# Kernel tuning notes

Hardware: AMD Instinct MI355X
Metric: run time of the kernel (lower is better)

Reference implementation:

```python
import jax, jax.numpy as jnp
import numpy as np

N = 50000
NEG_SLOPE = 0.2  # PyG GATConv default leaky_relu slope


def _gat_layer(x, src, dst, W, a_s, a_d, b):
    # x: [N, Fin]; W: [Fin, H*C]; a_s, a_d: [H, C]; b: [C]
    H, C = a_s.shape
    xp = (x @ W).reshape(N, H, C)                      # projected node features per head
    alpha_s = jnp.einsum('nhc,hc->nh', xp, a_s)        # [N, H]
    alpha_d = jnp.einsum('nhc,hc->nh', xp, a_d)        # [N, H]
    e = jax.nn.leaky_relu(alpha_s[src] + alpha_d[dst], NEG_SLOPE)  # [E, H]
    # segment softmax over incoming edges of each dst node
    m = jax.ops.segment_max(e, dst, num_segments=N)
    m = jnp.where(jnp.isfinite(m), m, 0.0)
    p = jnp.exp(e - jax.lax.stop_gradient(m)[dst])
    denom = jax.ops.segment_sum(p, dst, num_segments=N)
    alpha = p / denom[dst]                             # [E, H]
    # scatter-aggregate messages
    out = jax.ops.segment_sum(alpha[:, :, None] * xp[src], dst, num_segments=N)  # [N, H, C]
    return out.mean(axis=1) + b                        # concat=False -> mean over heads


def setup_inputs() -> dict:
    key = jax.random.key(0)
    ks = jax.random.split(key, 16)
    IN, HID, OUT, H = 128, 64, 40, 4
    E = 800000
    x = jax.random.normal(ks[0], (N, IN), dtype=jnp.float32)
    edge_index = jax.random.randint(ks[1], (2, E), 0, N, dtype=jnp.int64)

    def mk(kw, ka, fin, fout):
        s = 1.0 / np.sqrt(fin)
        W = jax.random.normal(kw, (fin, H * fout), dtype=jnp.float32) * s
        a_s = jax.random.normal(ka, (H, fout), dtype=jnp.float32) * 0.1
        a_d = jax.random.normal(jax.random.fold_in(ka, 1), (H, fout), dtype=jnp.float32) * 0.1
        b = jnp.zeros((fout,), dtype=jnp.float32)
        return W, a_s, a_d, b

    W1, as1, ad1, b1 = mk(ks[2], ks[3], IN, HID)
    W2, as2, ad2, b2 = mk(ks[4], ks[5], HID, HID)
    W3, as3, ad3, b3 = mk(ks[6], ks[7], HID, OUT)
    return dict(x=x, edge_index=edge_index,
                W1=W1, as1=as1, ad1=ad1, b1=b1,
                W2=W2, as2=as2, ad2=ad2, b2=b2,
                W3=W3, as3=as3, ad3=ad3, b3=b3)


def reference(x, edge_index, W1, as1, ad1, b1, W2, as2, ad2, b2, W3, as3, ad3, b3):
    # PyG GATConv adds self-loops by default
    loop = jnp.arange(N, dtype=edge_index.dtype)
    src = jnp.concatenate([edge_index[0], loop])
    dst = jnp.concatenate([edge_index[1], loop])
    h = jax.nn.relu(_gat_layer(x, src, dst, W1, as1, ad1, b1))   # dropout is identity in eval
    h = jax.nn.relu(_gat_layer(h, src, dst, W2, as2, ad2, b2))
    h = jax.nn.relu(_gat_layer(h, src, dst, W3, as3, ad3, b3))
    return jax.nn.log_softmax(h, axis=-1)
```

## Files before the change

kernel.cpp:

```cpp
#include <hip/hip_runtime.h>
#include <math.h>

#define NNODES 50000
#define NEG_SLOPE 0.2f

typedef unsigned short ushort8v __attribute__((ext_vector_type(8)));
typedef unsigned short ushort4v __attribute__((ext_vector_type(4)));
typedef short short8v __attribute__((ext_vector_type(8)));
typedef float f32x4 __attribute__((ext_vector_type(4)));
typedef float f32x2 __attribute__((ext_vector_type(2)));

__device__ __forceinline__ unsigned short f2bf(float f){
    unsigned u = __float_as_uint(f);
    u += 0x7fff + ((u >> 16) & 1);
    return (unsigned short)(u >> 16);
}

__global__ void init_kernel(const unsigned long long* __restrict__ e, int* __restrict__ flag,
                            int* __restrict__ deg, int N){
    if(blockIdx.x == 0 && threadIdx.x < 64){
        const unsigned long long v = e[threadIdx.x];
        const unsigned long long mask = __ballot(v >= (1ULL << 32));
        if(threadIdx.x == 0) *flag = (mask == 0ULL) ? 1 : 0;
    }
    for(int i = blockIdx.x * blockDim.x + threadIdx.x; i < N; i += gridDim.x * blockDim.x)
        deg[i] = 0;
}

__global__ void hist_kernel(const void* __restrict__ e, const int* __restrict__ flag,
                            int* __restrict__ deg, int E){
    const int i = blockIdx.x * blockDim.x + threadIdx.x;
    if(i < E){
        const int d = (*flag) ? (int)((const long long*)e)[E + i] : ((const int*)e)[E + i];
        atomicAdd(&deg[d], 1);
    }
}

__global__ __launch_bounds__(512) void scan1_kernel(const int* __restrict__ deg,
                                                    int* __restrict__ excl,
                                                    int* __restrict__ bsum, int n){
    __shared__ int sh[512];
    const int t = threadIdx.x;
    const int gid = blockIdx.x * 512 + t;
    const int v = (gid < n) ? deg[gid] : 0;
    sh[t] = v;
    __syncthreads();
    for(int off = 1; off < 512; off <<= 1){
        const int add = (t >= off) ? sh[t - off] : 0;
        __syncthreads();
        sh[t] += add;
        __syncthreads();
    }
    if(gid < n) excl[gid] = sh[t] - v;
    if(t == 511) bsum[blockIdx.x] = sh[511];
}

__global__ __launch_bounds__(128) void scan2_kernel(int* __restrict__ bsum, int nb){
    __shared__ int sh[128];
    const int t = threadIdx.x;
    const int v = (t < nb) ? bsum[t] : 0;
    sh[t] = v;
    __syncthreads();
    for(int off = 1; off < 128; off <<= 1){
        const int add = (t >= off) ? sh[t - off] : 0;
        __syncthreads();
        sh[t] += add;
        __syncthreads();
    }
    if(t < nb) bsum[t] = sh[t] - v;
}

__global__ void scan3_kernel(const int* __restrict__ excl, const int* __restrict__ bsum,
                             int* __restrict__ row_ptr, int* __restrict__ cursor,
                             int n, int E){
    const int gid = blockIdx.x * blockDim.x + threadIdx.x;
    if(gid < n){
        const int r = excl[gid] + bsum[gid >> 9];
        row_ptr[gid] = r;
        cursor[gid] = r;
    }
    if(gid == 0) row_ptr[n] = E;
}

__global__ void scatter_kernel(const void* __restrict__ e, const int* __restrict__ flag,
                               int* __restrict__ cursor, int* __restrict__ col, int E){
    const int i = blockIdx.x * blockDim.x + threadIdx.x;
    if(i < E){
        int s, d;
        if(*flag){ s = (int)((const long long*)e)[i]; d = (int)((const long long*)e)[E + i]; }
        else     { s = ((const int*)e)[i];            d = ((const int*)e)[E + i]; }
        const int pos = atomicAdd(&cursor[d], 1);
        col[pos] = s;
    }
}

__device__ __forceinline__ void emit_wa(const float* __restrict__ W, const float* __restrict__ a_s,
                                        const float* __restrict__ a_d, unsigned short* __restrict__ Wt,
                                        int Kin, int C, int id){
    const int n = id / Kin, k = id - n * Kin;
    float v = 0.f;
    if(n < 8){
        const int hh = n & 3;
        const float* av = (n < 4) ? a_s : a_d;
        for(int c = 0; c < C; c++) v += W[(size_t)k * (4 * C) + hh * C + c] * av[hh * C + c];
    }
    Wt[id] = f2bf(v);
}

__device__ __forceinline__ void emit_wc(const float* __restrict__ W, unsigned short* __restrict__ Wt,
                                        int Kin, int C, int id){
    const int c = id / (4 * Kin);
    const int hk = id - c * (4 * Kin);
    const int h = hk / Kin, k = hk - h * Kin;
    const float v = (c < C) ? W[(size_t)k * (4 * C) + h * C + c] * 0.25f : 0.f;
    Wt[id] = f2bf(v);
}

__global__ void prep_kernel(const float* __restrict__ x, unsigned short* __restrict__ xbf, int X4,
                            const float* __restrict__ W1, const float* __restrict__ as1, const float* __restrict__ ad1,
                            const float* __restrict__ W2, const float* __restrict__ as2, const float* __restrict__ ad2,
                            const float* __restrict__ W3, const float* __restrict__ as3, const float* __restrict__ ad3,
                            unsigned short* __restrict__ Wa1, unsigned short* __restrict__ Wa2,
                            unsigned short* __restrict__ Wa3, unsigned short* __restrict__ Wc1,
                            unsigned short* __restrict__ Wc2, unsigned short* __restrict__ Wc3){
    int id = blockIdx.x * blockDim.x + threadIdx.x;
    if(id < X4){
        const float4 v = *(const float4*)&x[(size_t)id * 4];
        ushort4v o;
        o[0] = f2bf(v.x); o[1] = f2bf(v.y); o[2] = f2bf(v.z); o[3] = f2bf(v.w);
        *(ushort4v*)&xbf[(size_t)id * 4] = o;
        return;
    }
    id -= X4;
    if(id < 16 * 128){ emit_wa(W1, as1, ad1, Wa1, 128, 64, id); return; }
    id -= 16 * 128;
    if(id < 16 * 64){ emit_wa(W2, as2, ad2, Wa2, 64, 64, id); return; }
    id -= 16 * 64;
    if(id < 16 * 64){ emit_wa(W3, as3, ad3, Wa3, 64, 40, id); return; }
    id -= 16 * 64;
    if(id < 64 * 512){ emit_wc(W1, Wc1, 128, 64, id); return; }
    id -= 64 * 512;
    if(id < 64 * 256){ emit_wc(W2, Wc2, 64, 64, id); return; }
    id -= 64 * 256;
    if(id < 48 * 256){ emit_wc(W3, Wc3, 64, 40, id); }
}

template<int K>
__global__ __launch_bounds__(256) void agemm_kernel(const unsigned short* __restrict__ A,
                                                    const unsigned short* __restrict__ Wa,
                                                    float* __restrict__ ea, float* __restrict__ ed,
                                                    int M){
    const int lane = threadIdx.x & 63;
    const int wave = threadIdx.x >> 6;
    const int quad = lane >> 4;
    const int l16 = lane & 15;
    const int bm = blockIdx.x * 64;
    const int m = min(bm + wave * 16 + l16, M - 1);
    f32x4 acc = {0,0,0,0};
    #pragma unroll
    for(int k0 = 0; k0 < K; k0 += 32){
        const short8v a = *(const short8v*)&A[(size_t)m * K + k0 + quad * 8];
        const short8v b = *(const short8v*)&Wa[(size_t)l16 * K + k0 + quad * 8];
        acc = __builtin_amdgcn_mfma_f32_16x16x32_bf16(a, b, acc, 0, 0, 0);
    }
    if(l16 < 8){
        const int h = l16 & 3;
        float* dst = (l16 < 4) ? ea : ed;
        const int rbase = bm + wave * 16 + quad * 4;
        #pragma unroll
        for(int r = 0; r < 4; r++){
            const int row = rbase + r;
            if(row < M){
                const float v = acc[r];
                *(f32x2*)&dst[(size_t)row * 8 + 2 * h] = (f32x2){__expf(v), __expf(NEG_SLOPE * v)};
            }
        }
    }
}

template<int K>
__global__ __launch_bounds__(256) void gather_kernel(const unsigned short* __restrict__ X,
                                                     const int* __restrict__ row_ptr,
                                                     const int* __restrict__ col,
                                                     const float* __restrict__ ea,
                                                     const float* __restrict__ ed,
                                                     unsigned short* __restrict__ g){
    constexpr int CPL = K / 16;
    constexpr int PAIRS = CPL / 2;
    const int lane = threadIdx.x & 63;
    const int wave = threadIdx.x >> 6;
    const int n = blockIdx.x * 4 + wave;
    const int slot = lane >> 4;
    const int pos = lane & 15;
    const int rs = row_ptr[n], re = row_ptr[n + 1];
    const int T = re - rs + 1;
    const float4 edA = *(const float4*)&ed[(size_t)n * 8];
    const float4 edB = *(const float4*)&ed[(size_t)n * 8 + 4];

    f32x2 acc[4][PAIRS];
    #pragma unroll
    for(int h = 0; h < 4; h++)
        #pragma unroll
        for(int p = 0; p < PAIRS; p++) acc[h][p] = (f32x2){0.f, 0.f};
    float dnm[4] = {0.f, 0.f, 0.f, 0.f};

    auto body = [&](int e){
        const int s = (e < re) ? col[e] : n;
        const float4 eaA = *(const float4*)&ea[(size_t)s * 8];
        const float4 eaB = *(const float4*)&ea[(size_t)s * 8 + 4];
        const float w0 = fmaxf(eaA.x * edA.x, eaA.y * edA.y);
        const float w1 = fmaxf(eaA.z * edA.z, eaA.w * edA.w);
        const float w2 = fmaxf(eaB.x * edB.x, eaB.y * edB.y);
        const float w3 = fmaxf(eaB.z * edB.z, eaB.w * edB.w);
        dnm[0] += w0; dnm[1] += w1; dnm[2] += w2; dnm[3] += w3;
        unsigned u[PAIRS];
        if constexpr(PAIRS == 2){
            const uint2 t2 = *(const uint2*)&X[(size_t)s * K + pos * CPL];
            u[0] = t2.x; u[1] = t2.y;
        } else {
            const uint4 t4 = *(const uint4*)&X[(size_t)s * K + pos * CPL];
            u[0] = t4.x; u[1] = t4.y; u[2] = t4.z; u[3] = t4.w;
        }
        #pragma unroll
        for(int p = 0; p < PAIRS; p++){
            const f32x2 v = {__uint_as_float(u[p] << 16), __uint_as_float(u[p] & 0xffff0000u)};
            acc[0][p] += (f32x2){w0, w0} * v;
            acc[1][p] += (f32x2){w1, w1} * v;
            acc[2][p] += (f32x2){w2, w2} * v;
            acc[3][p] += (f32x2){w3, w3} * v;
        }
    };

    int k = 0;
    for(; k + 8 <= T; k += 8){ body(rs + k + slot); body(rs + k + 4 + slot); }
    for(; k + 4 <= T; k += 4){ body(rs + k + slot); }
    if(k < T && slot < T - k){ body(rs + k + slot); }

    #pragma unroll
    for(int msk = 16; msk < 64; msk <<= 1){
        #pragma unroll
        for(int h = 0; h < 4; h++){
            #pragma unroll
            for(int p = 0; p < PAIRS; p++){
                acc[h][p][0] += __shfl_xor(acc[h][p][0], msk);
                acc[h][p][1] += __shfl_xor(acc[h][p][1], msk);
            }
            dnm[h] += __shfl_xor(dnm[h], msk);
        }
    }
    if(lane < 16){
        #pragma unroll
        for(int h = 0; h < 4; h++){
            const float sc = 1.f / dnm[h];
            if constexpr(PAIRS == 2){
                ushort4v o;
                o[0] = f2bf(acc[h][0][0] * sc); o[1] = f2bf(acc[h][0][1] * sc);
                o[2] = f2bf(acc[h][1][0] * sc); o[3] = f2bf(acc[h][1][1] * sc);
                *(ushort4v*)&g[(size_t)n * (4 * K) + h * K + pos * CPL] = o;
            } else {
                ushort8v o;
                #pragma unroll
                for(int p = 0; p < 4; p++){
                    o[2*p]   = f2bf(acc[h][p][0] * sc);
                    o[2*p+1] = f2bf(acc[h][p][1] * sc);
                }
                *(ushort8v*)&g[(size_t)n * (4 * K) + h * K + pos * CPL] = o;
            }
        }
    }
}

template<int KC, int NC, bool FINAL>
__global__ __launch_bounds__(256) void pgemm_kernel(const unsigned short* __restrict__ A,
                                                    const unsigned short* __restrict__ Bt,
                                                    const float* __restrict__ bias,
                                                    void* __restrict__ outv, int M){
    constexpr int NT = (NC + 15) / 16;
    const int lane = threadIdx.x & 63;
    const int wave = threadIdx.x >> 6;
    const int quad = lane >> 4;
    const int l16 = lane & 15;
    const int bm = blockIdx.x * 64;
    const int m = min(bm + wave * 16 + l16, M - 1);
    const size_t arow = (size_t)m * KC;

    f32x4 acc[NT];
    #pragma unroll
    for(int t = 0; t < NT; t++) acc[t] = (f32x4){0,0,0,0};

    for(int k0 = 0; k0 < KC; k0 += 32){
        const short8v a = *(const short8v*)&A[arow + k0 + quad * 8];
        #pragma unroll
        for(int t = 0; t < NT; t++){
            const short8v b = *(const short8v*)&Bt[(size_t)(t * 16 + l16) * KC + k0 + quad * 8];
            acc[t] = __builtin_amdgcn_mfma_f32_16x16x32_bf16(a, b, acc[t], 0, 0, 0);
        }
    }
    const int rbase = bm + wave * 16 + quad * 4;
    if(!FINAL){
        unsigned short* out = (unsigned short*)outv;
        #pragma unroll
        for(int t = 0; t < NT; t++){
            const int c = t * 16 + l16;
            #pragma unroll
            for(int r = 0; r < 4; r++){
                const int row = rbase + r;
                if(row < M) out[(size_t)row * NC + c] = f2bf(fmaxf(acc[t][r] + bias[c], 0.f));
            }
        }
    } else {
        float* out = (float*)outv;
        float o[NT][4];
        #pragma unroll
        for(int t = 0; t < NT; t++){
            const int c = t * 16 + l16;
            const bool valid = c < 40;
            const float bc = valid ? bias[c] : 0.f;
            #pragma unroll
            for(int r = 0; r < 4; r++)
                o[t][r] = valid ? fmaxf(acc[t][r] + bc, 0.f) : -INFINITY;
        }
        #pragma unroll
        for(int r = 0; r < 4; r++){
            float mx = o[0][r];
            #pragma unroll
            for(int t = 1; t < NT; t++) mx = fmaxf(mx, o[t][r]);
            #pragma unroll
            for(int off = 1; off < 16; off <<= 1) mx = fmaxf(mx, __shfl_xor(mx, off));
            float se = 0.f;
            #pragma unroll
            for(int t = 0; t < NT; t++) se += (o[t][r] > -INFINITY) ? __expf(o[t][r] - mx) : 0.f;
            #pragma unroll
            for(int off = 1; off < 16; off <<= 1) se += __shfl_xor(se, off);
            const float lz = mx + logf(se);
            const int row = rbase + r;
            if(row < M){
                #pragma unroll
                for(int t = 0; t < NT; t++){
                    const int c = t * 16 + l16;
                    if(c < 40) out[(size_t)row * 40 + c] = o[t][r] - lz;
                }
            }
        }
    }
}

extern "C" void kernel_launch(void* const* d_in, const int* in_sizes, int n_in,
                              void* d_out, int out_size, void* d_ws, size_t ws_size,
                              hipStream_t stream){
    const int N = NNODES;
    const int E = in_sizes[1] / 2;

    const float* x   = (const float*)d_in[0];
    const float* W1  = (const float*)d_in[2];
    const float* as1 = (const float*)d_in[3];
    const float* ad1 = (const float*)d_in[4];
    const float* b1  = (const float*)d_in[5];
    const float* W2  = (const float*)d_in[6];
    const float* as2 = (const float*)d_in[7];
    const float* ad2 = (const float*)d_in[8];
    const float* b2  = (const float*)d_in[9];
    const float* W3  = (const float*)d_in[10];
    const float* as3 = (const float*)d_in[11];
    const float* ad3 = (const float*)d_in[12];
    const float* b3  = (const float*)d_in[13];

    char* ws = (char*)d_ws;
    size_t off = 0;
    auto alloc = [&](size_t bytes) -> void* {
        void* p = ws + off;
        off = (off + bytes + 255) & ~(size_t)255;
        return p;
    };
    int*   flag    = (int*)  alloc(4);
    int*   row_ptr = (int*)  alloc((size_t)(N + 1) * 4);
    int*   colv    = (int*)  alloc((size_t)E * 4);
    int*   cursor  = (int*)  alloc((size_t)N * 4);
    int*   deg     = (int*)  alloc((size_t)N * 4);
    int*   excl    = (int*)  alloc((size_t)N * 4);
    int*   bsum    = (int*)  alloc(128 * 4);
    unsigned short* xbf = (unsigned short*)alloc((size_t)N * 128 * 2);
    unsigned short* Wa1 = (unsigned short*)alloc(16 * 128 * 2);
    unsigned short* Wa2 = (unsigned short*)alloc(16 * 64 * 2);
    unsigned short* Wa3 = (unsigned short*)alloc(16 * 64 * 2);
    unsigned short* Wc1 = (unsigned short*)alloc((size_t)64 * 512 * 2);
    unsigned short* Wc2 = (unsigned short*)alloc((size_t)64 * 256 * 2);
    unsigned short* Wc3 = (unsigned short*)alloc((size_t)48 * 256 * 2);
    float* eav     = (float*)alloc((size_t)N * 8 * 4);
    float* edv     = (float*)alloc((size_t)N * 8 * 4);
    unsigned short* g   = (unsigned short*)alloc((size_t)N * 512 * 2);
    unsigned short* h   = (unsigned short*)alloc((size_t)N * 64 * 2);
    (void)ws_size;

    const void* eraw = d_in[1];

    init_kernel<<<(N + 255) / 256, 256, 0, stream>>>((const unsigned long long*)eraw, flag, deg, N);
    hist_kernel<<<(E + 255) / 256, 256, 0, stream>>>(eraw, flag, deg, E);

    const int X4 = N * 128 / 4;
    const int prepTotal = X4 + 16*128 + 16*64 + 16*64 + 64*512 + 64*256 + 48*256;
    prep_kernel<<<(prepTotal + 255) / 256, 256, 0, stream>>>(x, xbf, X4,
                                                             W1, as1, ad1, W2, as2, ad2, W3, as3, ad3,
                                                             Wa1, Wa2, Wa3, Wc1, Wc2, Wc3);

    const int nbScan = (N + 511) / 512;
    scan1_kernel<<<nbScan, 512, 0, stream>>>(deg, excl, bsum, N);
    scan2_kernel<<<1, 128, 0, stream>>>(bsum, nbScan);
    scan3_kernel<<<(N + 255) / 256, 256, 0, stream>>>(excl, bsum, row_ptr, cursor, N, E);
    scatter_kernel<<<(E + 255) / 256, 256, 0, stream>>>(eraw, flag, cursor, colv, E);

    const int nodeBlocks = N / 4;
    const int mBlocks = (N + 63) / 64;

    agemm_kernel<128><<<mBlocks, 256, 0, stream>>>(xbf, Wa1, eav, edv, N);
    gather_kernel<128><<<nodeBlocks, 256, 0, stream>>>(xbf, row_ptr, colv, eav, edv, g);
    pgemm_kernel<512, 64, false><<<mBlocks, 256, 0, stream>>>(g, Wc1, b1, h, N);

    agemm_kernel<64><<<mBlocks, 256, 0, stream>>>(h, Wa2, eav, edv, N);
    gather_kernel<64><<<nodeBlocks, 256, 0, stream>>>(h, row_ptr, colv, eav, edv, g);
    pgemm_kernel<256, 64, false><<<mBlocks, 256, 0, stream>>>(g, Wc2, b2, h, N);

    agemm_kernel<64><<<mBlocks, 256, 0, stream>>>(h, Wa3, eav, edv, N);
    gather_kernel<64><<<nodeBlocks, 256, 0, stream>>>(h, row_ptr, colv, eav, edv, g);
    pgemm_kernel<256, 40, true><<<mBlocks, 256, 0, stream>>>(g, Wc3, b3, d_out, N);
}
```

Baseline: 436.3 us.

## Fuse gather aggregation with projection GEMM through shared memory

Merges the per-node attention gather kernel with the following projection GEMM. Each 1024-thread block now aggregates 16 nodes into LDS and then runs MFMA on that tile, with the bias, ReLU and final log-softmax applied in place. This removes the global round trip through the N×512 intermediate buffer and two kernel launches per layer. In exchange it uses 1024-thread blocks, where only NT waves do the GEMM while the rest sit idle, adds two block barriers, and uses more shared memory, which may lower occupancy. Two separate hidden buffers replace the in-place h, because the next agemm reads the previous layer's output.

```diff
diff --git a/kernel.cpp b/kernel.cpp
--- a/kernel.cpp
+++ b/kernel.cpp
@@ -178,18 +178,24 @@
     }
 }
 
-template<int K>
-__global__ __launch_bounds__(256) void gather_kernel(const unsigned short* __restrict__ X,
-                                                     const int* __restrict__ row_ptr,
-                                                     const int* __restrict__ col,
-                                                     const float* __restrict__ ea,
-                                                     const float* __restrict__ ed,
-                                                     unsigned short* __restrict__ g){
+template<int K, int NC, bool FINAL>
+__global__ __launch_bounds__(1024) void gatherp_kernel(const unsigned short* __restrict__ X,
+                                                       const int* __restrict__ row_ptr,
+                                                       const int* __restrict__ col,
+                                                       const float* __restrict__ ea,
+                                                       const float* __restrict__ ed,
+                                                       const unsigned short* __restrict__ Wc,
+                                                       const float* __restrict__ bias,
+                                                       void* __restrict__ outv){
+    constexpr int KC = 4 * K;
+    constexpr int NT = (NC + 15) / 16;
     constexpr int CPL = K / 16;
     constexpr int PAIRS = CPL / 2;
+    __shared__ unsigned short lg[16][KC + 8];
+    __shared__ float lo[16][NT * 16];
     const int lane = threadIdx.x & 63;
     const int wave = threadIdx.x >> 6;
-    const int n = blockIdx.x * 4 + wave;
+    const int n = blockIdx.x * 16 + wave;
     const int slot = lane >> 4;
     const int pos = lane & 15;
     const int rs = row_ptr[n], re = row_ptr[n + 1];
@@ -256,7 +262,7 @@
                 ushort4v o;
                 o[0] = f2bf(acc[h][0][0] * sc); o[1] = f2bf(acc[h][0][1] * sc);
                 o[2] = f2bf(acc[h][1][0] * sc); o[3] = f2bf(acc[h][1][1] * sc);
-                *(ushort4v*)&g[(size_t)n * (4 * K) + h * K + pos * CPL] = o;
+                *(ushort4v*)&lg[wave][h * K + pos * CPL] = o;
             } else {
                 ushort8v o;
                 #pragma unroll
@@ -264,84 +270,41 @@
                     o[2*p]   = f2bf(acc[h][p][0] * sc);
                     o[2*p+1] = f2bf(acc[h][p][1] * sc);
                 }
-                *(ushort8v*)&g[(size_t)n * (4 * K) + h * K + pos * CPL] = o;
+                *(ushort8v*)&lg[wave][h * K + pos * CPL] = o;
             }
         }
     }
-}
-
-template<int KC, int NC, bool FINAL>
-__global__ __launch_bounds__(256) void pgemm_kernel(const unsigned short* __restrict__ A,
-                                                    const unsigned short* __restrict__ Bt,
-                                                    const float* __restrict__ bias,
-                                                    void* __restrict__ outv, int M){
-    constexpr int NT = (NC + 15) / 16;
-    const int lane = threadIdx.x & 63;
-    const int wave = threadIdx.x >> 6;
-    const int quad = lane >> 4;
-    const int l16 = lane & 15;
-    const int bm = blockIdx.x * 64;
-    const int m = min(bm + wave * 16 + l16, M - 1);
-    const size_t arow = (size_t)m * KC;
-
-    f32x4 acc[NT];
-    #pragma unroll
-    for(int t = 0; t < NT; t++) acc[t] = (f32x4){0,0,0,0};
-
-    for(int k0 = 0; k0 < KC; k0 += 32){
-        const short8v a = *(const short8v*)&A[arow + k0 + quad * 8];
-        #pragma unroll
-        for(int t = 0; t < NT; t++){
-            const short8v b = *(const short8v*)&Bt[(size_t)(t * 16 + l16) * KC + k0 + quad * 8];
-            acc[t] = __builtin_amdgcn_mfma_f32_16x16x32_bf16(a, b, acc[t], 0, 0, 0);
-        }
-    }
-    const int rbase = bm + wave * 16 + quad * 4;
+    __syncthreads();
+
+    if(wave < NT){
+        const int quad = lane >> 4;
+        const int l16 = lane & 15;
+        f32x4 c4 = {0, 0, 0, 0};
+        for(int k0 = 0; k0 < KC; k0 += 32){
+            const short8v a = *(const short8v*)&lg[l16][k0 + quad * 8];
+            const short8v b = *(const short8v*)&Wc[(size_t)(wave * 16 + l16) * KC + k0 + quad * 8];
+            c4 = __builtin_amdgcn_mfma_f32_16x16x32_bf16(a, b, c4, 0, 0, 0);
+        }
+        #pragma unroll
+        for(int r = 0; r < 4; r++) lo[quad * 4 + r][wave * 16 + l16] = c4[r];
+    }
+    __syncthreads();
+
     if(!FINAL){
-        unsigned short* out = (unsigned short*)outv;
-        #pragma unroll
-        for(int t = 0; t < NT; t++){
-            const int c = t * 16 + l16;
-            #pragma unroll
-            for(int r = 0; r < 4; r++){
-                const int row = rbase + r;
-                if(row < M) out[(size_t)row * NC + c] = f2bf(fmaxf(acc[t][r] + bias[c], 0.f));
-            }
+        if(lane < NC){
+            const float o = fmaxf(lo[wave][lane] + bias[lane], 0.f);
+            ((unsigned short*)outv)[(size_t)n * NC + lane] = f2bf(o);
         }
     } else {
-        float* out = (float*)outv;
-        float o[NT][4];
-        #pragma unroll
-        for(int t = 0; t < NT; t++){
-            const int c = t * 16 + l16;
-            const bool valid = c < 40;
-            const float bc = valid ? bias[c] : 0.f;
-            #pragma unroll
-            for(int r = 0; r < 4; r++)
-                o[t][r] = valid ? fmaxf(acc[t][r] + bc, 0.f) : -INFINITY;
-        }
-        #pragma unroll
-        for(int r = 0; r < 4; r++){
-            float mx = o[0][r];
-            #pragma unroll
-            for(int t = 1; t < NT; t++) mx = fmaxf(mx, o[t][r]);
-            #pragma unroll
-            for(int off = 1; off < 16; off <<= 1) mx = fmaxf(mx, __shfl_xor(mx, off));
-            float se = 0.f;
-            #pragma unroll
-            for(int t = 0; t < NT; t++) se += (o[t][r] > -INFINITY) ? __expf(o[t][r] - mx) : 0.f;
-            #pragma unroll
-            for(int off = 1; off < 16; off <<= 1) se += __shfl_xor(se, off);
-            const float lz = mx + logf(se);
-            const int row = rbase + r;
-            if(row < M){
-                #pragma unroll
-                for(int t = 0; t < NT; t++){
-                    const int c = t * 16 + l16;
-                    if(c < 40) out[(size_t)row * 40 + c] = o[t][r] - lz;
-                }
-            }
-        }
+        const float o = (lane < 40) ? fmaxf(lo[wave][lane] + bias[lane], 0.f) : -INFINITY;
+        float mx = o;
+        #pragma unroll
+        for(int off = 1; off < 64; off <<= 1) mx = fmaxf(mx, __shfl_xor(mx, off));
+        float se = (lane < 40) ? __expf(o - mx) : 0.f;
+        #pragma unroll
+        for(int off = 1; off < 64; off <<= 1) se += __shfl_xor(se, off);
+        const float lz = mx + logf(se);
+        if(lane < 40) ((float*)outv)[(size_t)n * 40 + lane] = o - lz;
     }
 }
 
@@ -388,8 +351,8 @@
     unsigned short* Wc3 = (unsigned short*)alloc((size_t)48 * 256 * 2);
     float* eav     = (float*)alloc((size_t)N * 8 * 4);
     float* edv     = (float*)alloc((size_t)N * 8 * 4);
-    unsigned short* g   = (unsigned short*)alloc((size_t)N * 512 * 2);
-    unsigned short* h   = (unsigned short*)alloc((size_t)N * 64 * 2);
+    unsigned short* h1  = (unsigned short*)alloc((size_t)N * 64 * 2);
+    unsigned short* h2  = (unsigned short*)alloc((size_t)N * 64 * 2);
     (void)ws_size;
 
     const void* eraw = d_in[1];
@@ -409,18 +372,15 @@
     scan3_kernel<<<(N + 255) / 256, 256, 0, stream>>>(excl, bsum, row_ptr, cursor, N, E);
     scatter_kernel<<<(E + 255) / 256, 256, 0, stream>>>(eraw, flag, cursor, colv, E);
 
-    const int nodeBlocks = N / 4;
     const int mBlocks = (N + 63) / 64;
+    const int fBlocks = N / 16;
 
     agemm_kernel<128><<<mBlocks, 256, 0, stream>>>(xbf, Wa1, eav, edv, N);
-    gather_kernel<128><<<nodeBlocks, 256, 0, stream>>>(xbf, row_ptr, colv, eav, edv, g);
-    pgemm_kernel<512, 64, false><<<mBlocks, 256, 0, stream>>>(g, Wc1, b1, h, N);
-
-    agemm_kernel<64><<<mBlocks, 256, 0, stream>>>(h, Wa2, eav, edv, N);
-    gather_kernel<64><<<nodeBlocks, 256, 0, stream>>>(h, row_ptr, colv, eav, edv, g);
-    pgemm_kernel<256, 64, false><<<mBlocks, 256, 0, stream>>>(g, Wc2, b2, h, N);
-
-    agemm_kernel<64><<<mBlocks, 256, 0, stream>>>(h, Wa3, eav, edv, N);
-    gather_kernel<64><<<nodeBlocks, 256, 0, stream>>>(h, row_ptr, colv, eav, edv, g);
-    pgemm_kernel<256, 40, true><<<mBlocks, 256, 0, stream>>>(g, Wc3, b3, d_out, N);
-}
+    gatherp_kernel<128, 64, false><<<fBlocks, 1024, 0, stream>>>(xbf, row_ptr, colv, eav, edv, Wc1, b1, h1);
+
+    agemm_kernel<64><<<mBlocks, 256, 0, stream>>>(h1, Wa2, eav, edv, N);
+    gatherp_kernel<64, 64, false><<<fBlocks, 1024, 0, stream>>>(h1, row_ptr, colv, eav, edv, Wc2, b2, h2);
+
+    agemm_kernel<64><<<mBlocks, 256, 0, stream>>>(h2, Wa3, eav, edv, N);
+    gatherp_kernel<64, 40, true><<<fBlocks, 1024, 0, stream>>>(h2, row_ptr, colv, eav, edv, Wc3, b3, d_out);
+}
```

Result: slower. 497.4 us (+14.0%).

## Fuse attention-logit GEMM into projection GEMM epilogue and merge init with prep

Applied to the files above, without the earlier changes.

The next layer's attention-logit projection (agemm) now runs in the pgemm epilogue for layers 1 and 2. The bf16 ReLU output is staged in shared memory and multiplied by Wa with MFMA, and the exp terms are written to ea/ed directly. This removes two kernel launches and the re-read of h from global memory, and double-buffers h to avoid aliasing. It also merges the degree-zeroing init kernel into the prep kernel to save one launch. The cost is extra shared memory and epilogue work in pgemm.

```diff
diff --git a/kernel.cpp b/kernel.cpp
--- a/kernel.cpp
+++ b/kernel.cpp
@@ -16,15 +16,63 @@
     return (unsigned short)(u >> 16);
 }
 
-__global__ void init_kernel(const unsigned long long* __restrict__ e, int* __restrict__ flag,
-                            int* __restrict__ deg, int N){
+__device__ __forceinline__ void emit_wa(const float* __restrict__ W, const float* __restrict__ a_s,
+                                        const float* __restrict__ a_d, unsigned short* __restrict__ Wt,
+                                        int Kin, int C, int id){
+    const int n = id / Kin, k = id - n * Kin;
+    float v = 0.f;
+    if(n < 8){
+        const int hh = n & 3;
+        const float* av = (n < 4) ? a_s : a_d;
+        for(int c = 0; c < C; c++) v += W[(size_t)k * (4 * C) + hh * C + c] * av[hh * C + c];
+    }
+    Wt[id] = f2bf(v);
+}
+
+__device__ __forceinline__ void emit_wc(const float* __restrict__ W, unsigned short* __restrict__ Wt,
+                                        int Kin, int C, int id){
+    const int c = id / (4 * Kin);
+    const int hk = id - c * (4 * Kin);
+    const int h = hk / Kin, k = hk - h * Kin;
+    const float v = (c < C) ? W[(size_t)k * (4 * C) + h * C + c] * 0.25f : 0.f;
+    Wt[id] = f2bf(v);
+}
+
+__global__ void initprep_kernel(const unsigned long long* __restrict__ e, int* __restrict__ flag,
+                                int* __restrict__ deg, int N,
+                                const float* __restrict__ x, unsigned short* __restrict__ xbf, int X4,
+                                const float* __restrict__ W1, const float* __restrict__ as1, const float* __restrict__ ad1,
+                                const float* __restrict__ W2, const float* __restrict__ as2, const float* __restrict__ ad2,
+                                const float* __restrict__ W3, const float* __restrict__ as3, const float* __restrict__ ad3,
+                                unsigned short* __restrict__ Wa1, unsigned short* __restrict__ Wa2,
+                                unsigned short* __restrict__ Wa3, unsigned short* __restrict__ Wc1,
+                                unsigned short* __restrict__ Wc2, unsigned short* __restrict__ Wc3){
     if(blockIdx.x == 0 && threadIdx.x < 64){
         const unsigned long long v = e[threadIdx.x];
         const unsigned long long mask = __ballot(v >= (1ULL << 32));
         if(threadIdx.x == 0) *flag = (mask == 0ULL) ? 1 : 0;
     }
-    for(int i = blockIdx.x * blockDim.x + threadIdx.x; i < N; i += gridDim.x * blockDim.x)
-        deg[i] = 0;
+    int id = blockIdx.x * blockDim.x + threadIdx.x;
+    if(id < N) deg[id] = 0;
+    if(id < X4){
+        const float4 v = *(const float4*)&x[(size_t)id * 4];
+        ushort4v o;
+        o[0] = f2bf(v.x); o[1] = f2bf(v.y); o[2] = f2bf(v.z); o[3] = f2bf(v.w);
+        *(ushort4v*)&xbf[(size_t)id * 4] = o;
+        return;
+    }
+    id -= X4;
+    if(id < 16 * 128){ emit_wa(W1, as1, ad1, Wa1, 128, 64, id); return; }
+    id -= 16 * 128;
+    if(id < 16 * 64){ emit_wa(W2, as2, ad2, Wa2, 64, 64, id); return; }
+    id -= 16 * 64;
+    if(id < 16 * 64){ emit_wa(W3, as3, ad3, Wa3, 64, 40, id); return; }
+    id -= 16 * 64;
+    if(id < 64 * 512){ emit_wc(W1, Wc1, 128, 64, id); return; }
+    id -= 64 * 512;
+    if(id < 64 * 256){ emit_wc(W2, Wc2, 64, 64, id); return; }
+    id -= 64 * 256;
+    if(id < 48 * 256){ emit_wc(W3, Wc3, 64, 40, id); }
 }
 
 __global__ void hist_kernel(const void* __restrict__ e, const int* __restrict__ flag,
@@ -92,57 +140,6 @@
         const int pos = atomicAdd(&cursor[d], 1);
         col[pos] = s;
     }
-}
-
-__device__ __forceinline__ void emit_wa(const float* __restrict__ W, const float* __restrict__ a_s,
-                                        const float* __restrict__ a_d, unsigned short* __restrict__ Wt,
-                                        int Kin, int C, int id){
-    const int n = id / Kin, k = id - n * Kin;
-    float v = 0.f;
-    if(n < 8){
-        const int hh = n & 3;
-        const float* av = (n < 4) ? a_s : a_d;
-        for(int c = 0; c < C; c++) v += W[(size_t)k * (4 * C) + hh * C + c] * av[hh * C + c];
-    }
-    Wt[id] = f2bf(v);
-}
-
-__device__ __forceinline__ void emit_wc(const float* __restrict__ W, unsigned short* __restrict__ Wt,
-                                        int Kin, int C, int id){
-    const int c = id / (4 * Kin);
-    const int hk = id - c * (4 * Kin);
-    const int h = hk / Kin, k = hk - h * Kin;
-    const float v = (c < C) ? W[(size_t)k * (4 * C) + h * C + c] * 0.25f : 0.f;
-    Wt[id] = f2bf(v);
-}
-
-__global__ void prep_kernel(const float* __restrict__ x, unsigned short* __restrict__ xbf, int X4,
-                            const float* __restrict__ W1, const float* __restrict__ as1, const float* __restrict__ ad1,
-                            const float* __restrict__ W2, const float* __restrict__ as2, const float* __restrict__ ad2,
-                            const float* __restrict__ W3, const float* __restrict__ as3, const float* __restrict__ ad3,
-                            unsigned short* __restrict__ Wa1, unsigned short* __restrict__ Wa2,
-                            unsigned short* __restrict__ Wa3, unsigned short* __restrict__ Wc1,
-                            unsigned short* __restrict__ Wc2, unsigned short* __restrict__ Wc3){
-    int id = blockIdx.x * blockDim.x + threadIdx.x;
-    if(id < X4){
-        const float4 v = *(const float4*)&x[(size_t)id * 4];
-        ushort4v o;
-        o[0] = f2bf(v.x); o[1] = f2bf(v.y); o[2] = f2bf(v.z); o[3] = f2bf(v.w);
-        *(ushort4v*)&xbf[(size_t)id * 4] = o;
-        return;
-    }
-    id -= X4;
-    if(id < 16 * 128){ emit_wa(W1, as1, ad1, Wa1, 128, 64, id); return; }
-    id -= 16 * 128;
-    if(id < 16 * 64){ emit_wa(W2, as2, ad2, Wa2, 64, 64, id); return; }
-    id -= 16 * 64;
-    if(id < 16 * 64){ emit_wa(W3, as3, ad3, Wa3, 64, 40, id); return; }
-    id -= 16 * 64;
-    if(id < 64 * 512){ emit_wc(W1, Wc1, 128, 64, id); return; }
-    id -= 64 * 512;
-    if(id < 64 * 256){ emit_wc(W2, Wc2, 64, 64, id); return; }
-    id -= 64 * 256;
-    if(id < 48 * 256){ emit_wc(W3, Wc3, 64, 40, id); }
 }
 
 template<int K>
@@ -270,12 +267,17 @@
     }
 }
 
-template<int KC, int NC, bool FINAL>
+template<int KC, int NC, bool FINAL, bool ALPHA>
 __global__ __launch_bounds__(256) void pgemm_kernel(const unsigned short* __restrict__ A,
                                                     const unsigned short* __restrict__ Bt,
                                                     const float* __restrict__ bias,
-                                                    void* __restrict__ outv, int M){
+                                                    void* __restrict__ outv,
+                                                    const unsigned short* __restrict__ Wa,
+                                                    float* __restrict__ ea,
+                                                    float* __restrict__ ed,
+                                                    int M){
     constexpr int NT = (NC + 15) / 16;
+    __shared__ unsigned short lh[ALPHA ? 4 : 1][16][72];
     const int lane = threadIdx.x & 63;
     const int wave = threadIdx.x >> 6;
     const int quad = lane >> 4;
@@ -304,8 +306,31 @@
             const int c = t * 16 + l16;
             #pragma unroll
             for(int r = 0; r < 4; r++){
+                const unsigned short hb = f2bf(fmaxf(acc[t][r] + bias[c], 0.f));
                 const int row = rbase + r;
-                if(row < M) out[(size_t)row * NC + c] = f2bf(fmaxf(acc[t][r] + bias[c], 0.f));
+                if(row < M) out[(size_t)row * NC + c] = hb;
+                if constexpr(ALPHA) lh[wave][quad * 4 + r][c] = hb;
+            }
+        }
+        if constexpr(ALPHA){
+            f32x4 a4 = {0, 0, 0, 0};
+            #pragma unroll
+            for(int k0 = 0; k0 < 64; k0 += 32){
+                const short8v a = *(const short8v*)&lh[wave][l16][k0 + quad * 8];
+                const short8v b = *(const short8v*)&Wa[(size_t)l16 * 64 + k0 + quad * 8];
+                a4 = __builtin_amdgcn_mfma_f32_16x16x32_bf16(a, b, a4, 0, 0, 0);
+            }
+            if(l16 < 8){
+                const int h = l16 & 3;
+                float* dst = (l16 < 4) ? ea : ed;
+                #pragma unroll
+                for(int r = 0; r < 4; r++){
+                    const int row = rbase + r;
+                    if(row < M){
+                        const float v = a4[r];
+                        *(f32x2*)&dst[(size_t)row * 8 + 2 * h] = (f32x2){__expf(v), __expf(NEG_SLOPE * v)};
+                    }
+                }
             }
         }
     } else {
@@ -389,20 +414,20 @@
     float* eav     = (float*)alloc((size_t)N * 8 * 4);
     float* edv     = (float*)alloc((size_t)N * 8 * 4);
     unsigned short* g   = (unsigned short*)alloc((size_t)N * 512 * 2);
-    unsigned short* h   = (unsigned short*)alloc((size_t)N * 64 * 2);
+    unsigned short* h1  = (unsigned short*)alloc((size_t)N * 64 * 2);
+    unsigned short* h2  = (unsigned short*)alloc((size_t)N * 64 * 2);
     (void)ws_size;
 
     const void* eraw = d_in[1];
-
-    init_kernel<<<(N + 255) / 256, 256, 0, stream>>>((const unsigned long long*)eraw, flag, deg, N);
-    hist_kernel<<<(E + 255) / 256, 256, 0, stream>>>(eraw, flag, deg, E);
 
     const int X4 = N * 128 / 4;
     const int prepTotal = X4 + 16*128 + 16*64 + 16*64 + 64*512 + 64*256 + 48*256;
-    prep_kernel<<<(prepTotal + 255) / 256, 256, 0, stream>>>(x, xbf, X4,
-                                                             W1, as1, ad1, W2, as2, ad2, W3, as3, ad3,
-                                                             Wa1, Wa2, Wa3, Wc1, Wc2, Wc3);
-
+    initprep_kernel<<<(prepTotal + 255) / 256, 256, 0, stream>>>(
+        (const unsigned long long*)eraw, flag, deg, N, x, xbf, X4,
+        W1, as1, ad1, W2, as2, ad2, W3, as3, ad3,
+        Wa1, Wa2, Wa3, Wc1, Wc2, Wc3);
+
+    hist_kernel<<<(E + 255) / 256, 256, 0, stream>>>(eraw, flag, deg, E);
     const int nbScan = (N + 511) / 512;
     scan1_kernel<<<nbScan, 512, 0, stream>>>(deg, excl, bsum, N);
     scan2_kernel<<<1, 128, 0, stream>>>(bsum, nbScan);
@@ -414,13 +439,11 @@
 
     agemm_kernel<128><<<mBlocks, 256, 0, stream>>>(xbf, Wa1, eav, edv, N);
     gather_kernel<128><<<nodeBlocks, 256, 0, stream>>>(xbf, row_ptr, colv, eav, edv, g);
-    pgemm_kernel<512, 64, false><<<mBlocks, 256, 0, stream>>>(g, Wc1, b1, h, N);
-
-    agemm_kernel<64><<<mBlocks, 256, 0, stream>>>(h, Wa2, eav, edv, N);
-    gather_kernel<64><<<nodeBlocks, 256, 0, stream>>>(h, row_ptr, colv, eav, edv, g);
-    pgemm_kernel<256, 64, false><<<mBlocks, 256, 0, stream>>>(g, Wc2, b2, h, N);
-
-    agemm_kernel<64><<<mBlocks, 256, 0, stream>>>(h, Wa3, eav, edv, N);
-    gather_kernel<64><<<nodeBlocks, 256, 0, stream>>>(h, row_ptr, colv, eav, edv, g);
-    pgemm_kernel<256, 40, true><<<mBlocks, 256, 0, stream>>>(g, Wc3, b3, d_out, N);
-}
+    pgemm_kernel<512, 64, false, true><<<mBlocks, 256, 0, stream>>>(g, Wc1, b1, h1, Wa2, eav, edv, N);
+
+    gather_kernel<64><<<nodeBlocks, 256, 0, stream>>>(h1, row_ptr, colv, eav, edv, g);
+    pgemm_kernel<256, 64, false, true><<<mBlocks, 256, 0, stream>>>(g, Wc2, b2, h2, Wa3, eav, edv, N);
+
+    gather_kernel<64><<<nodeBlocks, 256, 0, stream>>>(h2, row_ptr, colv, eav, edv, g);
+    pgemm_kernel<256, 40, true, false><<<mBlocks, 256, 0, stream>>>(g, Wc3, b3, d_out, nullptr, nullptr, nullptr, N);
+}
```

Result: faster. 421.9 us, median of 2 (-3.3%).
